# Kernel tuning notes

Measured on AMD Instinct MI355X. Metric: run time of the kernel, lower is better.

Reference implementation:

```python
import jax, jax.numpy as jnp
import numpy as np

# module constants (match init_kwargs)
D_MODEL = 1024
N_HEADS = 16
D_K = 64
CHUNK_LEN = 64
EPS = 1e-8

B, C, N, NL = 4, 16, 2, 128  # batch, chunks, neighbors, neighbor_len
S = C * CHUNK_LEN            # seq_len = 1024


def setup_inputs() -> dict:
    key = jax.random.key(0)
    ks = jax.random.split(key, 10)
    s = 0.02
    HD = N_HEADS * D_K
    return {
        "h": jax.random.normal(ks[0], (B, S, D_MODEL), jnp.float32),
        "e": jax.random.normal(ks[1], (B, C, N, NL, D_MODEL), jnp.float32),
        "g_norm": jnp.ones((D_MODEL,), jnp.float32),
        "Wq": jax.random.normal(ks[2], (D_MODEL, HD), jnp.float32) * s,
        "bq": jnp.zeros((HD,), jnp.float32),
        "Wk": jax.random.normal(ks[3], (D_MODEL, HD), jnp.float32) * s,
        "bk": jnp.zeros((HD,), jnp.float32),
        "Wv": jax.random.normal(ks[4], (D_MODEL, HD), jnp.float32) * s,
        "bv": jnp.zeros((HD,), jnp.float32),
        "Wo": jax.random.normal(ks[5], (HD, D_MODEL), jnp.float32) * s,
        "bo": jnp.zeros((D_MODEL,), jnp.float32),
    }


def _rmsnorm(x, g):
    return x * g * jax.lax.rsqrt(jnp.mean(x * x, axis=-1, keepdims=True) + EPS)


def reference(h, e, g_norm, Wq, bq, Wk, bk, Wv, bv, Wo, bo):
    b, seq, d = h.shape
    _, c, n, nl, _ = e.shape
    cl = CHUNK_LEN
    scale = 1.0 / np.sqrt(D_K).astype(np.float32)

    h_res = h
    hn = _rmsnorm(h[:, cl - 1:], g_norm)                 # [b, seq-cl+1, d]
    pad = c * cl - hn.shape[1]
    hn = jnp.pad(hn, ((0, 0), (0, pad), (0, 0)))         # [b, c*cl, d]
    hn = hn.reshape(b, c, cl, d)

    q = (hn @ Wq + bq).reshape(b, c, cl, N_HEADS, D_K)       # bcihd
    k = (e @ Wk + bk).reshape(b, c, n, nl, N_HEADS, D_K)     # bcnjhd
    v = (e @ Wv + bv).reshape(b, c, n, nl, N_HEADS, D_K)

    attn = jnp.einsum('bcihd,bcnjhd->bchinj', q, k) * scale  # [b,c,h,i,n,j]
    attn = jax.nn.softmax(attn.reshape(b, c, N_HEADS, cl, n * nl), axis=-1)
    attn = attn.reshape(b, c, N_HEADS, cl, n, nl)

    o = jnp.einsum('bchinj,bcnjhd->bcihd', attn, v)
    o = o.reshape(b, c * cl, N_HEADS * D_K)
    o = o @ Wo + bo                                          # [b, c*cl, d]
    o = jnp.pad(o, ((0, 0), (cl - 1, 0), (0, 0)))            # shift right by cl-1
    return o[:, :seq] + h_res
```

## Files before the change

### kernel.cpp

```cpp
#include <hip/hip_runtime.h>
#include <stdint.h>

#define DEV __device__ __forceinline__

typedef __attribute__((ext_vector_type(8))) __bf16 bf16x8;
typedef __attribute__((ext_vector_type(4))) float floatx4;

DEV float bf2f(unsigned short u) {
  union { unsigned int i; float f; } x; x.i = ((unsigned int)u) << 16; return x.f;
}
DEV unsigned int f2bf(float f) {
  union { float f; unsigned int i; } x; x.f = f;
  unsigned int r = x.i + 0x7FFFu + ((x.i >> 16) & 1u);
  return r >> 16;
}
DEV void gl2lds16(const unsigned short* g, unsigned short* l) {
  __builtin_amdgcn_global_load_lds(
      (const __attribute__((address_space(1))) unsigned int*)g,
      (__attribute__((address_space(3))) unsigned int*)l, 16, 0, 0);
}
DEV floatx4 zero4() { floatx4 z; z[0]=0.f; z[1]=0.f; z[2]=0.f; z[3]=0.f; return z; }

__global__ void cca_transpose_k(const float* __restrict__ W0,
                                const float* __restrict__ W1,
                                const float* __restrict__ W2,
                                const float* __restrict__ W3,
                                unsigned short* __restrict__ D0,
                                unsigned short* __restrict__ D1,
                                unsigned short* __restrict__ D2,
                                unsigned short* __restrict__ D3) {
  __shared__ float tile[64][65];
  const float* W; unsigned short* Wt;
  switch (blockIdx.z) {
    case 0: W = W0; Wt = D0; break;
    case 1: W = W1; Wt = D1; break;
    case 2: W = W2; Wt = D2; break;
    default: W = W3; Wt = D3; break;
  }
  const int K = 1024, N = 1024;
  int k0 = blockIdx.x * 64, n0 = blockIdx.y * 64;
  int t = threadIdx.x;
  int c = t & 63, r4 = t >> 6;
#pragma unroll
  for (int it = 0; it < 16; ++it) {
    int r = it * 4 + r4;
    tile[r][c] = W[(size_t)(k0 + r) * N + n0 + c];
  }
  __syncthreads();
#pragma unroll
  for (int it = 0; it < 16; ++it) {
    int r = it * 4 + r4;
    Wt[(size_t)(n0 + r) * K + k0 + c] = (unsigned short)f2bf(tile[c][r]);
  }
}

__global__ void cca_prep_k(const float* __restrict__ e,
                           unsigned short* __restrict__ eb,
                           const float* __restrict__ h,
                           const float* __restrict__ g,
                           unsigned short* __restrict__ hn,
                           float* __restrict__ out) {
  int blk = blockIdx.x;
  int t = threadIdx.x;
  if (blk < 16384) {
    int i = blk * 256 + t;
    float4 v = ((const float4*)e)[i];
    uint2 o;
    o.x = f2bf(v.x) | (f2bf(v.y) << 16);
    o.y = f2bf(v.z) | (f2bf(v.w) << 16);
    ((uint2*)eb)[i] = o;
    return;
  }
  if (blk < 20480) {
    int row = blk - 16384;
    int b = row >> 10, p = row & 1023;
    unsigned short* dst = hn + (size_t)row * 1024;
    if (p >= 961) {
      uint2 z; z.x = 0u; z.y = 0u;
      ((uint2*)dst)[t] = z;
      return;
    }
    const float* src = h + ((size_t)(b << 10) + p + 63) * 1024;
    float4 v = ((const float4*)src)[t];
    float ss = v.x*v.x + v.y*v.y + v.z*v.z + v.w*v.w;
#pragma unroll
    for (int m = 32; m > 0; m >>= 1) ss += __shfl_down(ss, m);
    __shared__ float wsum[4];
    int lane = t & 63, wv = t >> 6;
    if (lane == 0) wsum[wv] = ss;
    __syncthreads();
    float tot = wsum[0] + wsum[1] + wsum[2] + wsum[3];
    float r = rsqrtf(tot * (1.0f / 1024.0f) + 1e-8f);
    float4 gv = ((const float4*)g)[t];
    uint2 outp;
    outp.x = f2bf(v.x * gv.x * r) | (f2bf(v.y * gv.y * r) << 16);
    outp.y = f2bf(v.z * gv.z * r) | (f2bf(v.w * gv.w * r) << 16);
    ((uint2*)dst)[t] = outp;
    return;
  }
  {
    int idx = (blk - 20480) * 256 + t;
    const int n4 = 4 * 63 * 1024 / 4;
    if (idx < n4) {
      int e4 = idx * 4;
      int b = e4 / (63 * 1024);
      int r = e4 - b * (63 * 1024);
      size_t off = (size_t)b * 1024 * 1024 + (size_t)r;
      *(float4*)(out + off) = *(const float4*)(h + off);
    }
  }
}

template <int MODE>
__launch_bounds__(256, 2)
__global__ void cca_gemm_k(const unsigned short* __restrict__ A,
                           const unsigned short* __restrict__ Bt,
                           const float* __restrict__ bias1,
                           const float* __restrict__ bias2,
                           const float* __restrict__ resid,
                           void* __restrict__ Cout,
                           int M, int N, int K) {
  __shared__ unsigned short Ash[128 * 32];
  __shared__ unsigned short Bsh[128 * 32];
  int tM = blockIdx.x * 128, tN = blockIdx.y * 128;
  int t = threadIdx.x, lane = t & 63, wv = t >> 6;
  int wm = wv >> 1, wn = wv & 1;
  int l15 = lane & 15, quad = lane >> 4;
  int arow = lane >> 2, achk = lane & 3;
  int gchk = achk ^ ((arow >> 1) & 3);
  int rchk = quad ^ ((l15 >> 1) & 3);
  floatx4 acc[4][4];
#pragma unroll
  for (int i = 0; i < 4; ++i)
#pragma unroll
    for (int j = 0; j < 4; ++j) acc[i][j] = zero4();

  for (int k0 = 0; k0 < K; k0 += 32) {
    __syncthreads();
#pragma unroll
    for (int ii = 0; ii < 2; ++ii) {
      int seg = wv + ii * 4;
      int row = seg * 16 + arow;
      gl2lds16(A + (size_t)(tM + row) * K + k0 + gchk * 8, Ash + seg * 512);
      gl2lds16(Bt + (size_t)(tN + row) * K + k0 + gchk * 8, Bsh + seg * 512);
    }
    __syncthreads();
    bf16x8 af[4], bfv[4];
#pragma unroll
    for (int mt = 0; mt < 4; ++mt)
      af[mt] = *(const bf16x8*)&Ash[(wm * 64 + mt * 16 + l15) * 32 + rchk * 8];
#pragma unroll
    for (int nt = 0; nt < 4; ++nt)
      bfv[nt] = *(const bf16x8*)&Bsh[(wn * 64 + nt * 16 + l15) * 32 + rchk * 8];
#pragma unroll
    for (int mt = 0; mt < 4; ++mt)
#pragma unroll
      for (int nt = 0; nt < 4; ++nt)
        acc[mt][nt] = __builtin_amdgcn_mfma_f32_16x16x32_bf16(af[mt], bfv[nt], acc[mt][nt], 0, 0, 0);
  }

#pragma unroll
  for (int mt = 0; mt < 4; ++mt) {
    int mrow = tM + wm * 64 + mt * 16 + quad * 4;
#pragma unroll
    for (int nt = 0; nt < 4; ++nt) {
      int ncol = tN + wn * 64 + nt * 16 + l15;
      float bs;
      if (MODE == 0) {
        bs = (bias2 != nullptr && ncol >= 1024) ? bias2[ncol - 1024] : bias1[ncol];
      } else {
        bs = bias1[ncol];
      }
#pragma unroll
      for (int r = 0; r < 4; ++r) {
        int m = mrow + r;
        float v = acc[mt][nt][r] + bs;
        if (MODE == 0) {
          ((unsigned short*)Cout)[(size_t)m * N + ncol] = (unsigned short)f2bf(v);
        } else {
          int p = m & 1023;
          if (p < 961) {
            size_t o = (size_t)(m + 63) * 1024 + (size_t)ncol;
            ((float*)Cout)[o] = v + resid[o];
          }
        }
      }
    }
  }
}

__global__ void cca_vt_k(const unsigned short* __restrict__ KV,
                         unsigned short* __restrict__ VTb) {
  __shared__ unsigned short tile[256 * 66];
  int bch = blockIdx.x;
  int hh = bch & 15, c = (bch >> 4) & 15, b = bch >> 8;
  size_t kvbase = (size_t)b * 4096 + (size_t)c * 256;
  int t = threadIdx.x;
#pragma unroll
  for (int it = 0; it < 16; ++it) {
    int flat = it * 256 + t;
    int row = flat >> 4, cu = flat & 15;
    uint2 v = *(const uint2*)(KV + (kvbase + row) * 2048 + 1024 + hh * 64 + cu * 4);
    int d0 = cu * 4;
    tile[row * 66 + d0 + 0] = (unsigned short)(v.x & 0xffff);
    tile[row * 66 + d0 + 1] = (unsigned short)(v.x >> 16);
    tile[row * 66 + d0 + 2] = (unsigned short)(v.y & 0xffff);
    tile[row * 66 + d0 + 3] = (unsigned short)(v.y >> 16);
  }
  __syncthreads();
  unsigned short* dst = VTb + (size_t)bch * 16384;
#pragma unroll
  for (int it = 0; it < 16; ++it) {
    int flat = it * 256 + t;
    int d = flat >> 6, ju = flat & 63;
    int j = ju * 4;
    unsigned int lo = (unsigned int)tile[(j + 0) * 66 + d] |
                      ((unsigned int)tile[(j + 1) * 66 + d] << 16);
    unsigned int hi = (unsigned int)tile[(j + 2) * 66 + d] |
                      ((unsigned int)tile[(j + 3) * 66 + d] << 16);
    int u = j >> 3, joff = j & 7;
    int phys = d * 256 + ((u ^ (d & 7)) << 3) + joff;
    uint2 o; o.x = lo; o.y = hi;
    *(uint2*)(dst + phys) = o;
  }
}

__launch_bounds__(256, 2)
__global__ void cca_attn_k(const unsigned short* __restrict__ Q,
                           const unsigned short* __restrict__ KV,
                           const unsigned short* __restrict__ VTb,
                           unsigned short* __restrict__ O) {
  __shared__ unsigned short smemA[64 * 64 + 256 * 64];
  __shared__ unsigned short VTlds[64 * 256];
  unsigned short* Qsh = smemA;
  unsigned short* Ksh = smemA + 64 * 64;
  unsigned short* Psh = smemA;
  int bch = blockIdx.x;
  int hh = bch & 15, c = (bch >> 4) & 15, b = bch >> 8;
  int t = threadIdx.x, lane = t & 63, wv = t >> 6;
  int l15 = lane & 15, quad = lane >> 4;
  size_t qbase = (size_t)b * 1024 + (size_t)c * 64;
  size_t kvbase = (size_t)b * 4096 + (size_t)c * 256;
  int hoff = hh * 64;

  {
    int rowi = lane >> 3, chk = lane & 7;
#pragma unroll
    for (int ii = 0; ii < 2; ++ii) {
      int seg = wv + ii * 4;
      int row = seg * 8 + rowi;
      gl2lds16(Q + (qbase + row) * 1024 + hoff + chk * 8, Qsh + seg * 512);
    }
#pragma unroll
    for (int ii = 0; ii < 8; ++ii) {
      int seg = wv + ii * 4;
      int row = seg * 8 + rowi;
      gl2lds16(KV + (kvbase + row) * 2048 + hoff + chk * 8, Ksh + seg * 512);
    }
    const unsigned short* vsrc = VTb + (size_t)bch * 16384;
#pragma unroll
    for (int ii = 0; ii < 8; ++ii) {
      int seg = wv + ii * 4;
      gl2lds16(vsrc + seg * 512 + lane * 8, VTlds + seg * 512);
    }
  }
  __syncthreads();

  floatx4 st[16];
#pragma unroll
  for (int i = 0; i < 16; ++i) st[i] = zero4();
  bf16x8 a0 = *(const bf16x8*)&Qsh[(wv * 16 + l15) * 64 + quad * 8];
  bf16x8 a1 = *(const bf16x8*)&Qsh[(wv * 16 + l15) * 64 + 32 + quad * 8];
#pragma unroll
  for (int kt = 0; kt < 16; ++kt) {
    bf16x8 b0 = *(const bf16x8*)&Ksh[(kt * 16 + l15) * 64 + quad * 8];
    bf16x8 b1 = *(const bf16x8*)&Ksh[(kt * 16 + l15) * 64 + 32 + quad * 8];
    st[kt] = __builtin_amdgcn_mfma_f32_16x16x32_bf16(a0, b0, st[kt], 0, 0, 0);
    st[kt] = __builtin_amdgcn_mfma_f32_16x16x32_bf16(a1, b1, st[kt], 0, 0, 0);
  }
  __syncthreads();

  const float scale = 0.125f;
#pragma unroll
  for (int r = 0; r < 4; ++r) {
    float mx = -1e30f;
#pragma unroll
    for (int kt = 0; kt < 16; ++kt) mx = fmaxf(mx, st[kt][r]);
    mx = fmaxf(mx, __shfl_xor(mx, 1));
    mx = fmaxf(mx, __shfl_xor(mx, 2));
    mx = fmaxf(mx, __shfl_xor(mx, 4));
    mx = fmaxf(mx, __shfl_xor(mx, 8));
    float sum = 0.f;
#pragma unroll
    for (int kt = 0; kt < 16; ++kt) {
      float e = __expf((st[kt][r] - mx) * scale);
      st[kt][r] = e;
      sum += e;
    }
    sum += __shfl_xor(sum, 1);
    sum += __shfl_xor(sum, 2);
    sum += __shfl_xor(sum, 4);
    sum += __shfl_xor(sum, 8);
    float inv = 1.0f / sum;
    int prow = wv * 16 + quad * 4 + r;
#pragma unroll
    for (int kt = 0; kt < 16; ++kt)
      Psh[prow * 264 + kt * 16 + l15] = (unsigned short)f2bf(st[kt][r] * inv);
  }

  floatx4 ot[4];
#pragma unroll
  for (int nt = 0; nt < 4; ++nt) ot[nt] = zero4();
#pragma unroll
  for (int kt2 = 0; kt2 < 8; ++kt2) {
    bf16x8 ap = *(const bf16x8*)&Psh[(wv * 16 + l15) * 264 + kt2 * 32 + quad * 8];
#pragma unroll
    for (int nt = 0; nt < 4; ++nt) {
      int vrow = nt * 16 + l15;
      int u = kt2 * 4 + quad;
      bf16x8 bv8 = *(const bf16x8*)&VTlds[vrow * 256 + ((u ^ (vrow & 7)) << 3)];
      ot[nt] = __builtin_amdgcn_mfma_f32_16x16x32_bf16(ap, bv8, ot[nt], 0, 0, 0);
    }
  }
#pragma unroll
  for (int nt = 0; nt < 4; ++nt) {
#pragma unroll
    for (int r = 0; r < 4; ++r) {
      int i = wv * 16 + quad * 4 + r;
      int dcol = hoff + nt * 16 + l15;
      O[(qbase + i) * 1024 + dcol] = (unsigned short)f2bf(ot[nt][r]);
    }
  }
}

extern "C" void kernel_launch(void* const* d_in, const int* in_sizes, int n_in,
                              void* d_out, int out_size, void* d_ws, size_t ws_size,
                              hipStream_t stream) {
  const float* h  = (const float*)d_in[0];
  const float* e  = (const float*)d_in[1];
  const float* g  = (const float*)d_in[2];
  const float* Wq = (const float*)d_in[3];
  const float* bq = (const float*)d_in[4];
  const float* Wk = (const float*)d_in[5];
  const float* bk = (const float*)d_in[6];
  const float* Wv = (const float*)d_in[7];
  const float* bv = (const float*)d_in[8];
  const float* Wo = (const float*)d_in[9];
  const float* bo = (const float*)d_in[10];
  float* out = (float*)d_out;

  unsigned short* ws   = (unsigned short*)d_ws;
  unsigned short* hn   = ws;
  unsigned short* WqT  = hn   + (size_t)4096 * 1024;
  unsigned short* WkvT = WqT  + (size_t)1024 * 1024;
  unsigned short* WoT  = WkvT + (size_t)2048 * 1024;
  unsigned short* Qb   = WoT  + (size_t)1024 * 1024;
  unsigned short* KVb  = Qb   + (size_t)4096 * 1024;
  unsigned short* Ob   = KVb  + (size_t)16384 * 2048;
  unsigned short* eb   = Ob   + (size_t)4096 * 1024;
  unsigned short* VTb  = eb;

  cca_transpose_k<<<dim3(16, 16, 4), 256, 0, stream>>>(
      Wq, Wk, Wv, Wo, WqT, WkvT, WkvT + (size_t)1024 * 1024, WoT);

  cca_prep_k<<<20732, 256, 0, stream>>>(e, eb, h, g, hn, out);

  cca_gemm_k<0><<<dim3(32, 8), 256, 0, stream>>>(hn, WqT, bq, nullptr, nullptr,
                                                 (void*)Qb, 4096, 1024, 1024);
  cca_gemm_k<0><<<dim3(128, 16), 256, 0, stream>>>(eb, WkvT, bk, bv, nullptr,
                                                   (void*)KVb, 16384, 2048, 1024);

  cca_vt_k<<<1024, 256, 0, stream>>>(KVb, VTb);

  cca_attn_k<<<1024, 256, 0, stream>>>(Qb, KVb, VTb, Ob);

  cca_gemm_k<1><<<dim3(32, 8), 256, 0, stream>>>(Ob, WoT, bo, nullptr, h,
                                                 (void*)out, 4096, 1024, 1024);
}
```

Before: 313.0 us.

## Merge prep launches, fuse Q/KV GEMMs, deepen K tile, narrow output GEMM tile

The weight transpose is folded into the prep kernel and the Q and KV projection GEMMs are merged into one launch, which cuts launch count and tail effects. The GEMM K-step grows from 32 to 64 with a new 8-chunk XOR swizzle, halving the number of barrier pairs per tile at the cost of doubled LDS per block. The output-projection GEMM switches to 128x64 tiles, doubling its grid to 512 blocks for better CU coverage on the small M=4096 problem. The larger LDS footprint may lower occupancy, and the new swizzle mapping must stay correct.

```diff
diff --git a/kernel.cpp b/kernel.cpp
--- a/kernel.cpp
+++ b/kernel.cpp
@@ -6,9 +6,6 @@
 typedef __attribute__((ext_vector_type(8))) __bf16 bf16x8;
 typedef __attribute__((ext_vector_type(4))) float floatx4;
 
-DEV float bf2f(unsigned short u) {
-  union { unsigned int i; float f; } x; x.i = ((unsigned int)u) << 16; return x.f;
-}
 DEV unsigned int f2bf(float f) {
   union { float f; unsigned int i; } x; x.f = f;
   unsigned int r = x.i + 0x7FFFu + ((x.i >> 16) & 1u);
@@ -21,49 +18,41 @@
 }
 DEV floatx4 zero4() { floatx4 z; z[0]=0.f; z[1]=0.f; z[2]=0.f; z[3]=0.f; return z; }
 
-__global__ void cca_transpose_k(const float* __restrict__ W0,
-                                const float* __restrict__ W1,
-                                const float* __restrict__ W2,
-                                const float* __restrict__ W3,
-                                unsigned short* __restrict__ D0,
-                                unsigned short* __restrict__ D1,
-                                unsigned short* __restrict__ D2,
-                                unsigned short* __restrict__ D3) {
+__global__ void cca_prep_k(const float* __restrict__ W0, const float* __restrict__ W1,
+                           const float* __restrict__ W2, const float* __restrict__ W3,
+                           unsigned short* __restrict__ D0, unsigned short* __restrict__ D1,
+                           unsigned short* __restrict__ D2, unsigned short* __restrict__ D3,
+                           const float* __restrict__ e, unsigned short* __restrict__ eb,
+                           const float* __restrict__ h, const float* __restrict__ g,
+                           unsigned short* __restrict__ hn, float* __restrict__ out) {
   __shared__ float tile[64][65];
-  const float* W; unsigned short* Wt;
-  switch (blockIdx.z) {
-    case 0: W = W0; Wt = D0; break;
-    case 1: W = W1; Wt = D1; break;
-    case 2: W = W2; Wt = D2; break;
-    default: W = W3; Wt = D3; break;
-  }
-  const int K = 1024, N = 1024;
-  int k0 = blockIdx.x * 64, n0 = blockIdx.y * 64;
-  int t = threadIdx.x;
-  int c = t & 63, r4 = t >> 6;
-#pragma unroll
-  for (int it = 0; it < 16; ++it) {
-    int r = it * 4 + r4;
-    tile[r][c] = W[(size_t)(k0 + r) * N + n0 + c];
-  }
-  __syncthreads();
-#pragma unroll
-  for (int it = 0; it < 16; ++it) {
-    int r = it * 4 + r4;
-    Wt[(size_t)(n0 + r) * K + k0 + c] = (unsigned short)f2bf(tile[c][r]);
-  }
-}
-
-__global__ void cca_prep_k(const float* __restrict__ e,
-                           unsigned short* __restrict__ eb,
-                           const float* __restrict__ h,
-                           const float* __restrict__ g,
-                           unsigned short* __restrict__ hn,
-                           float* __restrict__ out) {
   int blk = blockIdx.x;
   int t = threadIdx.x;
-  if (blk < 16384) {
-    int i = blk * 256 + t;
+  if (blk < 1024) {
+    const float* W; unsigned short* Wt;
+    switch (blk >> 8) {
+      case 0: W = W0; Wt = D0; break;
+      case 1: W = W1; Wt = D1; break;
+      case 2: W = W2; Wt = D2; break;
+      default: W = W3; Wt = D3; break;
+    }
+    int k0 = (blk & 15) * 64, n0 = ((blk >> 4) & 15) * 64;
+    int c = t & 63, r4 = t >> 6;
+#pragma unroll
+    for (int it = 0; it < 16; ++it) {
+      int r = it * 4 + r4;
+      tile[r][c] = W[(size_t)(k0 + r) * 1024 + n0 + c];
+    }
+    __syncthreads();
+#pragma unroll
+    for (int it = 0; it < 16; ++it) {
+      int r = it * 4 + r4;
+      Wt[(size_t)(n0 + r) * 1024 + k0 + c] = (unsigned short)f2bf(tile[c][r]);
+    }
+    return;
+  }
+  if (blk < 17408) {
+    int i = (blk - 1024) * 256 + t;
     float4 v = ((const float4*)e)[i];
     uint2 o;
     o.x = f2bf(v.x) | (f2bf(v.y) << 16);
@@ -71,8 +60,8 @@
     ((uint2*)eb)[i] = o;
     return;
   }
-  if (blk < 20480) {
-    int row = blk - 16384;
+  if (blk < 21504) {
+    int row = blk - 17408;
     int b = row >> 10, p = row & 1023;
     unsigned short* dst = hn + (size_t)row * 1024;
     if (p >= 961) {
@@ -99,7 +88,7 @@
     return;
   }
   {
-    int idx = (blk - 20480) * 256 + t;
+    int idx = (blk - 21504) * 256 + t;
     const int n4 = 4 * 63 * 1024 / 4;
     if (idx < n4) {
       int e4 = idx * 4;
@@ -111,52 +100,70 @@
   }
 }
 
-template <int MODE>
 __launch_bounds__(256, 2)
-__global__ void cca_gemm_k(const unsigned short* __restrict__ A,
-                           const unsigned short* __restrict__ Bt,
-                           const float* __restrict__ bias1,
-                           const float* __restrict__ bias2,
-                           const float* __restrict__ resid,
-                           void* __restrict__ Cout,
-                           int M, int N, int K) {
-  __shared__ unsigned short Ash[128 * 32];
-  __shared__ unsigned short Bsh[128 * 32];
-  int tM = blockIdx.x * 128, tN = blockIdx.y * 128;
+__global__ void cca_gemmQKV_k(const unsigned short* __restrict__ eb,
+                              const unsigned short* __restrict__ WkvT,
+                              const float* __restrict__ bk,
+                              const float* __restrict__ bv,
+                              unsigned short* __restrict__ KVb,
+                              const unsigned short* __restrict__ hn,
+                              const unsigned short* __restrict__ WqT,
+                              const float* __restrict__ bq,
+                              unsigned short* __restrict__ Qb) {
+  __shared__ unsigned short Ash[128 * 64];
+  __shared__ unsigned short Bsh[128 * 64];
+  int blk = blockIdx.x;
+  const unsigned short *A, *Bt; const float *b1, *b2; unsigned short* C;
+  int N, tM, tN;
+  if (blk < 2048) {
+    A = eb; Bt = WkvT; b1 = bk; b2 = bv; C = KVb; N = 2048;
+    tM = (blk & 127) * 128; tN = (blk >> 7) * 128;
+  } else {
+    int q = blk - 2048;
+    A = hn; Bt = WqT; b1 = bq; b2 = nullptr; C = Qb; N = 1024;
+    tM = (q & 31) * 128; tN = (q >> 5) * 128;
+  }
   int t = threadIdx.x, lane = t & 63, wv = t >> 6;
   int wm = wv >> 1, wn = wv & 1;
   int l15 = lane & 15, quad = lane >> 4;
-  int arow = lane >> 2, achk = lane & 3;
-  int gchk = achk ^ ((arow >> 1) & 3);
-  int rchk = quad ^ ((l15 >> 1) & 3);
+  int arow = lane >> 3, achk = lane & 7;
+  int gchk = achk ^ arow;
   floatx4 acc[4][4];
 #pragma unroll
   for (int i = 0; i < 4; ++i)
 #pragma unroll
     for (int j = 0; j < 4; ++j) acc[i][j] = zero4();
 
-  for (int k0 = 0; k0 < K; k0 += 32) {
-    __syncthreads();
-#pragma unroll
-    for (int ii = 0; ii < 2; ++ii) {
-      int seg = wv + ii * 4;
-      int row = seg * 16 + arow;
-      gl2lds16(A + (size_t)(tM + row) * K + k0 + gchk * 8, Ash + seg * 512);
-      gl2lds16(Bt + (size_t)(tN + row) * K + k0 + gchk * 8, Bsh + seg * 512);
-    }
-    __syncthreads();
-    bf16x8 af[4], bfv[4];
-#pragma unroll
-    for (int mt = 0; mt < 4; ++mt)
-      af[mt] = *(const bf16x8*)&Ash[(wm * 64 + mt * 16 + l15) * 32 + rchk * 8];
-#pragma unroll
-    for (int nt = 0; nt < 4; ++nt)
-      bfv[nt] = *(const bf16x8*)&Bsh[(wn * 64 + nt * 16 + l15) * 32 + rchk * 8];
-#pragma unroll
-    for (int mt = 0; mt < 4; ++mt)
-#pragma unroll
-      for (int nt = 0; nt < 4; ++nt)
-        acc[mt][nt] = __builtin_amdgcn_mfma_f32_16x16x32_bf16(af[mt], bfv[nt], acc[mt][nt], 0, 0, 0);
+  for (int k0 = 0; k0 < 1024; k0 += 64) {
+    __syncthreads();
+#pragma unroll
+    for (int ii = 0; ii < 4; ++ii) {
+      int seg = ii * 4 + wv;
+      int row = seg * 8 + arow;
+      gl2lds16(A + (size_t)(tM + row) * 1024 + k0 + gchk * 8, Ash + seg * 512);
+      gl2lds16(Bt + (size_t)(tN + row) * 1024 + k0 + gchk * 8, Bsh + seg * 512);
+    }
+    __syncthreads();
+#pragma unroll
+    for (int h = 0; h < 2; ++h) {
+      int u = (h << 2) | quad;
+      bf16x8 af[4], bfv[4];
+#pragma unroll
+      for (int mt = 0; mt < 4; ++mt) {
+        int r = wm * 64 + mt * 16 + l15;
+        af[mt] = *(const bf16x8*)&Ash[r * 64 + ((u ^ (l15 & 7)) << 3)];
+      }
+#pragma unroll
+      for (int nt = 0; nt < 4; ++nt) {
+        int r = wn * 64 + nt * 16 + l15;
+        bfv[nt] = *(const bf16x8*)&Bsh[r * 64 + ((u ^ (l15 & 7)) << 3)];
+      }
+#pragma unroll
+      for (int mt = 0; mt < 4; ++mt)
+#pragma unroll
+        for (int nt = 0; nt < 4; ++nt)
+          acc[mt][nt] = __builtin_amdgcn_mfma_f32_16x16x32_bf16(af[mt], bfv[nt], acc[mt][nt], 0, 0, 0);
+    }
   }
 
 #pragma unroll
@@ -165,24 +172,87 @@
 #pragma unroll
     for (int nt = 0; nt < 4; ++nt) {
       int ncol = tN + wn * 64 + nt * 16 + l15;
-      float bs;
-      if (MODE == 0) {
-        bs = (bias2 != nullptr && ncol >= 1024) ? bias2[ncol - 1024] : bias1[ncol];
-      } else {
-        bs = bias1[ncol];
-      }
+      float bs = (b2 != nullptr && ncol >= 1024) ? b2[ncol - 1024] : b1[ncol];
 #pragma unroll
       for (int r = 0; r < 4; ++r) {
         int m = mrow + r;
-        float v = acc[mt][nt][r] + bs;
-        if (MODE == 0) {
-          ((unsigned short*)Cout)[(size_t)m * N + ncol] = (unsigned short)f2bf(v);
-        } else {
-          int p = m & 1023;
-          if (p < 961) {
-            size_t o = (size_t)(m + 63) * 1024 + (size_t)ncol;
-            ((float*)Cout)[o] = v + resid[o];
-          }
+        C[(size_t)m * N + ncol] = (unsigned short)f2bf(acc[mt][nt][r] + bs);
+      }
+    }
+  }
+}
+
+__launch_bounds__(256, 2)
+__global__ void cca_gemmO_k(const unsigned short* __restrict__ A,
+                            const unsigned short* __restrict__ Bt,
+                            const float* __restrict__ bias,
+                            const float* __restrict__ resid,
+                            float* __restrict__ out) {
+  __shared__ unsigned short Ash[128 * 64];
+  __shared__ unsigned short Bsh[64 * 64];
+  int tM = blockIdx.x * 128, tN = blockIdx.y * 64;
+  int t = threadIdx.x, lane = t & 63, wv = t >> 6;
+  int wm = wv >> 1, wn = wv & 1;
+  int l15 = lane & 15, quad = lane >> 4;
+  int arow = lane >> 3, achk = lane & 7;
+  int gchk = achk ^ arow;
+  floatx4 acc[4][2];
+#pragma unroll
+  for (int i = 0; i < 4; ++i)
+#pragma unroll
+    for (int j = 0; j < 2; ++j) acc[i][j] = zero4();
+
+  for (int k0 = 0; k0 < 1024; k0 += 64) {
+    __syncthreads();
+#pragma unroll
+    for (int ii = 0; ii < 4; ++ii) {
+      int seg = ii * 4 + wv;
+      int row = seg * 8 + arow;
+      gl2lds16(A + (size_t)(tM + row) * 1024 + k0 + gchk * 8, Ash + seg * 512);
+    }
+#pragma unroll
+    for (int ii = 0; ii < 2; ++ii) {
+      int seg = ii * 4 + wv;
+      int row = seg * 8 + arow;
+      gl2lds16(Bt + (size_t)(tN + row) * 1024 + k0 + gchk * 8, Bsh + seg * 512);
+    }
+    __syncthreads();
+#pragma unroll
+    for (int h = 0; h < 2; ++h) {
+      int u = (h << 2) | quad;
+      bf16x8 af[4], bfv[2];
+#pragma unroll
+      for (int mt = 0; mt < 4; ++mt) {
+        int r = wm * 64 + mt * 16 + l15;
+        af[mt] = *(const bf16x8*)&Ash[r * 64 + ((u ^ (l15 & 7)) << 3)];
+      }
+#pragma unroll
+      for (int nt = 0; nt < 2; ++nt) {
+        int r = wn * 32 + nt * 16 + l15;
+        bfv[nt] = *(const bf16x8*)&Bsh[r * 64 + ((u ^ (l15 & 7)) << 3)];
+      }
+#pragma unroll
+      for (int mt = 0; mt < 4; ++mt)
+#pragma unroll
+        for (int nt = 0; nt < 2; ++nt)
+          acc[mt][nt] = __builtin_amdgcn_mfma_f32_16x16x32_bf16(af[mt], bfv[nt], acc[mt][nt], 0, 0, 0);
+    }
+  }
+
+#pragma unroll
+  for (int mt = 0; mt < 4; ++mt) {
+    int mrow = tM + wm * 64 + mt * 16 + quad * 4;
+#pragma unroll
+    for (int nt = 0; nt < 2; ++nt) {
+      int ncol = tN + wn * 32 + nt * 16 + l15;
+      float bs = bias[ncol];
+#pragma unroll
+      for (int r = 0; r < 4; ++r) {
+        int m = mrow + r;
+        int p = m & 1023;
+        if (p < 961) {
+          size_t o = (size_t)(m + 63) * 1024 + (size_t)ncol;
+          out[o] = acc[mt][nt][r] + bs + resid[o];
         }
       }
     }
@@ -360,20 +430,16 @@
   unsigned short* eb   = Ob   + (size_t)4096 * 1024;
   unsigned short* VTb  = eb;
 
-  cca_transpose_k<<<dim3(16, 16, 4), 256, 0, stream>>>(
-      Wq, Wk, Wv, Wo, WqT, WkvT, WkvT + (size_t)1024 * 1024, WoT);
-
-  cca_prep_k<<<20732, 256, 0, stream>>>(e, eb, h, g, hn, out);
-
-  cca_gemm_k<0><<<dim3(32, 8), 256, 0, stream>>>(hn, WqT, bq, nullptr, nullptr,
-                                                 (void*)Qb, 4096, 1024, 1024);
-  cca_gemm_k<0><<<dim3(128, 16), 256, 0, stream>>>(eb, WkvT, bk, bv, nullptr,
-                                                   (void*)KVb, 16384, 2048, 1024);
+  cca_prep_k<<<21756, 256, 0, stream>>>(
+      Wq, Wk, Wv, Wo, WqT, WkvT, WkvT + (size_t)1024 * 1024, WoT,
+      e, eb, h, g, hn, out);
+
+  cca_gemmQKV_k<<<2304, 256, 0, stream>>>(eb, WkvT, bk, bv, KVb,
+                                          hn, WqT, bq, Qb);
 
   cca_vt_k<<<1024, 256, 0, stream>>>(KVb, VTb);
 
   cca_attn_k<<<1024, 256, 0, stream>>>(Qb, KVb, VTb, Ob);
 
-  cca_gemm_k<1><<<dim3(32, 8), 256, 0, stream>>>(Ob, WoT, bo, nullptr, h,
-                                                 (void*)out, 4096, 1024, 1024);
-}
+  cca_gemmO_k<<<dim3(32, 16), 256, 0, stream>>>(Ob, WoT, bo, h, out);
+}
```

Measured after the change: 275.1 us. 1.14x faster.
